# Optimization experiments

Hardware: AMD Instinct MI355X
Metric: run time of the kernel (lower is better)

The kernel has to match this reference:

```python
import jax, jax.numpy as jnp
import numpy as np

BIN_SIZE = 128
DIST_MULT = 0.1
LN_EPS = 1e-6


def setup_inputs() -> dict:
    key = jax.random.key(0)
    ks = jax.random.split(key, 24)
    B, N, D, DD, H = 8, 25600, 256, 128, 128
    s = 0.02
    inp = {
        'x': jax.random.normal(ks[0], (B, N, D), dtype=jnp.float32),
        'msk': jax.random.randint(ks[1], (B, N), 0, 2) > 0,
        'ln_g': jnp.ones((D,), jnp.float32),
        'ln_b': jnp.zeros((D,), jnp.float32),
        # ffn_dist: Linear(256,128) ELU Linear(128,128) ELU Linear(128,128)
        'w1': s * jax.random.normal(ks[2], (D, H), jnp.float32),
        'b1': jnp.zeros((H,), jnp.float32),
        'w2': s * jax.random.normal(ks[3], (H, H), jnp.float32),
        'b2': jnp.zeros((H,), jnp.float32),
        'w3': s * jax.random.normal(ks[4], (H, DD), jnp.float32),
        'b3': jnp.zeros((DD,), jnp.float32),
        # LSH codebook random rotations [distance_dim, max_num_bins//2]
        'codebook': jax.random.normal(ks[5], (DD, 100), jnp.float32),
        # two GHConvDense layers, hidden_dim=output_dim=256
        'theta0': jax.random.normal(ks[6], (D, D), jnp.float32) * s,
        'wh0': jax.random.normal(ks[7], (D, D), jnp.float32) * s,
        'wt0': jax.random.normal(ks[8], (D, D), jnp.float32) * s,
        'bt0': jnp.zeros((D,), jnp.float32),
        'theta1': jax.random.normal(ks[9], (D, D), jnp.float32) * s,
        'wh1': jax.random.normal(ks[10], (D, D), jnp.float32) * s,
        'wt1': jax.random.normal(ks[11], (D, D), jnp.float32) * s,
        'bt1': jnp.zeros((D,), jnp.float32),
    }
    return inp


def _forward(x, msk, ln_g, ln_b, w1, b1, w2, b2, w3, b3, codebook,
             theta0, wh0, wt0, bt0, theta1, wh1, wt1, bt1):
    B, n_elems, D = x.shape
    pad = (-n_elems) % BIN_SIZE  # static python int
    if pad:
        x = jnp.pad(x, ((0, 0), (0, pad), (0, 0)))
        msk = jnp.pad(msk, ((0, 0), (0, pad)), constant_values=True)
    Np = n_elems + pad
    n_bins = Np // BIN_SIZE

    # layernorm
    mu = jnp.mean(x, -1, keepdims=True)
    var = jnp.mean(jnp.square(x - mu), -1, keepdims=True)
    xn = (x - mu) * jax.lax.rsqrt(var + LN_EPS) * ln_g + ln_b

    # distance FFN + dist activation (elu)
    h = jax.nn.elu(xn @ w1 + b1)
    h = jax.nn.elu(h @ w2 + b2)
    x_dist = jax.nn.elu(h @ w3 + b3)  # [B, Np, distance_dim]

    # LSH binning
    mul = x_dist @ codebook[:, :max(1, n_bins // 2)]
    cmul = jnp.concatenate([mul, -mul], axis=-1)  # [B, Np, n_bins]
    a = jnp.argmax(cmul, axis=-1)
    bin_idx = a + jnp.where(msk, 0, n_bins - 1)
    bins_split = jnp.argsort(bin_idx, axis=-1)  # [B, Np]

    # gather into bins
    xm = jnp.take_along_axis(x_dist, bins_split[..., None], axis=1)
    xm = xm.reshape(B, n_bins, BIN_SIZE, x_dist.shape[-1])
    xb = jnp.take_along_axis(xn, bins_split[..., None], axis=1)
    xb = xb.reshape(B, n_bins, BIN_SIZE, D)
    mskf = jnp.take_along_axis(msk, bins_split, axis=1)
    mskf = mskf.reshape(B, n_bins, BIN_SIZE, 1).astype(x.dtype)

    # pairwise Gaussian kernel within each bin
    xk = xm * mskf
    nsq = jnp.sum(jnp.square(xk), -1)  # [B, nb, P]
    inner = jnp.einsum('bnpd,bnqd->bnpq', xk, xk)
    d2 = nsq[..., :, None] - 2.0 * inner + nsq[..., None, :]
    dist = jnp.sqrt(jnp.clip(d2, 1e-6, 1e6))
    dm = jnp.clip(jnp.exp(-DIST_MULT * dist), 0.0, 1.0)
    dm = dm * mskf * jnp.swapaxes(mskf, -1, -2)  # mask rows & cols [B,nb,P,P]

    # gated graph convolutions
    for th, wh, wt, bt in ((theta0, wh0, wt0, bt0), (theta1, wh1, wt1, bt1)):
        xmk = xb * mskf
        f_hom = jnp.einsum('bnpq,bnqd->bnpd', dm, (xmk @ th) * mskf)
        f_het = xmk @ wh
        gate = jax.nn.sigmoid(xb @ wt + bt)
        xb = jax.nn.elu(gate * f_hom + (1.0 - gate) * f_het) * mskf

    # reverse LSH scatter
    xb_flat = xb.reshape(B, Np, D)
    ret = jax.vmap(lambda idx, pts: jnp.zeros((Np, D), pts.dtype).at[idx].set(pts))(
        bins_split, xb_flat)
    return ret[:, :n_elems, :]


def reference(x, msk, ln_g, ln_b, w1, b1, w2, b2, w3, b3, codebook,
              theta0, wh0, wt0, bt0, theta1, wh1, wt1, bt1):
    return _forward(x, msk, ln_g, ln_b, w1, b1, w2, b2, w3, b3, codebook,
                    theta0, wh0, wt0, bt0, theta1, wh1, wt1, bt1)
```

## Files before the change

### kernel.cpp

```cpp
#include <hip/hip_runtime.h>
#include <math.h>

#define B_ 8
#define NP_ 25600
#define T_ (B_*NP_)
#define D_ 256
#define H_ 128
#define DD_ 128
#define NBINS_ 200
#define NIDS_ 400
#define PB_ 128
#define NC_ 100
#define GT_ (B_*NBINS_)

typedef __attribute__((ext_vector_type(8))) short bf16x8;
typedef __attribute__((ext_vector_type(4))) float f32x4;
typedef __attribute__((ext_vector_type(4))) unsigned short u16x4;
typedef unsigned short u16;

__device__ __forceinline__ float eluf(float v){ return v > 0.f ? v : expm1f(v); }
__device__ __forceinline__ u16 f2bf(float f){
  union { float f; unsigned u; } v; v.f = f;
  unsigned r = v.u + 0x7fffu + ((v.u >> 16) & 1u);
  return (u16)(r >> 16);
}
__device__ __forceinline__ float bf2f(u16 h){
  union { unsigned u; float f; } v; v.u = ((unsigned)h) << 16; return v.f;
}

__device__ __forceinline__ void gl16(void* lds, const void* g){
  __builtin_amdgcn_global_load_lds((const __attribute__((address_space(1))) void*)g,
                                   (__attribute__((address_space(3))) void*)lds, 16, 0, 0);
}

__global__ void k_mask_detect(const unsigned int* __restrict__ m, int* __restrict__ flags){
  int any_f1 = 0, any_o = 0;
  for (int i = blockIdx.x*blockDim.x + threadIdx.x; i < T_/4; i += gridDim.x*blockDim.x){
    unsigned int w = m[i];
    if (w == 0x3F800000u) any_f1 = 1;
    else if (w > 1u) any_o = 1;
  }
  if (any_f1) atomicOr(&flags[0], 1);
  if (any_o)  atomicOr(&flags[1], 1);
}

__global__ void k_mask_convert(const void* __restrict__ m, const int* __restrict__ flags,
                               float* __restrict__ mskf){
  int i = blockIdx.x*256 + threadIdx.x;
  int mode = flags[0] ? 2 : (flags[1] ? 1 : 0);
  bool v;
  if (mode == 2)      v = ((const float*)m)[i] != 0.f;
  else if (mode == 1) v = ((const unsigned char*)m)[i] != 0;
  else                v = ((const int*)m)[i] != 0;
  mskf[i] = v ? 1.f : 0.f;
}

__global__ __launch_bounds__(256) void k_ln(const float* __restrict__ x,
    const float* __restrict__ g, const float* __restrict__ b, float* __restrict__ xn){
  const int wave = threadIdx.x >> 6, lane = threadIdx.x & 63;
  const long t = (long)blockIdx.x*4 + wave;
  float4 v = ((const float4*)(x + t*D_))[lane];
  float s  = v.x + v.y + v.z + v.w;
  float s2 = v.x*v.x + v.y*v.y + v.z*v.z + v.w*v.w;
  #pragma unroll
  for (int o = 32; o; o >>= 1){ s += __shfl_xor(s, o); s2 += __shfl_xor(s2, o); }
  const float mu = s * (1.f/D_);
  float var = s2*(1.f/D_) - mu*mu;
  var = fmaxf(var, 0.f);
  const float rs = rsqrtf(var + 1e-6f);
  float4 gg = ((const float4*)g)[lane];
  float4 bb = ((const float4*)b)[lane];
  float4 o4;
  o4.x = (v.x-mu)*rs*gg.x + bb.x;
  o4.y = (v.y-mu)*rs*gg.y + bb.y;
  o4.z = (v.z-mu)*rs*gg.z + bb.z;
  o4.w = (v.w-mu)*rs*gg.w + bb.w;
  ((float4*)(xn + t*D_))[lane] = o4;
}

template<int K>
__global__ __launch_bounds__(256) void k_gemm2(const float* __restrict__ A,
    const float* __restrict__ W, const float* __restrict__ bias, float* __restrict__ C){
  __shared__ __align__(16) float As[32*132];
  __shared__ __align__(16) float Bs[32*132];
  const size_t m0 = (size_t)blockIdx.x * 128;
  const int tid = threadIdx.x;
  const int tm = tid >> 4, tn = tid & 15;
  float acc[8][8] = {};
  for (int kc = 0; kc < K; kc += 32){
    __syncthreads();
    {
      const int r = tid >> 1, kq = (tid & 1) * 16;
      const float* src = &A[(m0 + r)*(size_t)K + kc + kq];
      #pragma unroll
      for (int q = 0; q < 4; ++q){
        const float4 v = ((const float4*)src)[q];
        As[(kq + q*4 + 0)*132 + r] = v.x;
        As[(kq + q*4 + 1)*132 + r] = v.y;
        As[(kq + q*4 + 2)*132 + r] = v.z;
        As[(kq + q*4 + 3)*132 + r] = v.w;
      }
      const int kk = tid >> 3, n0 = (tid & 7) * 16;
      const float* wsrc = &W[(size_t)(kc + kk)*128 + n0];
      #pragma unroll
      for (int q = 0; q < 4; ++q)
        *(float4*)&Bs[kk*132 + n0 + q*4] = ((const float4*)wsrc)[q];
    }
    __syncthreads();
    #pragma unroll
    for (int k = 0; k < 32; ++k){
      float a[8], b[8];
      *(float4*)&a[0] = *(const float4*)&As[k*132 + tm*4];
      *(float4*)&a[4] = *(const float4*)&As[k*132 + 64 + tm*4];
      *(float4*)&b[0] = *(const float4*)&Bs[k*132 + tn*4];
      *(float4*)&b[4] = *(const float4*)&Bs[k*132 + 64 + tn*4];
      #pragma unroll
      for (int i = 0; i < 8; ++i)
        #pragma unroll
        for (int j = 0; j < 8; ++j)
          acc[i][j] = fmaf(a[i], b[j], acc[i][j]);
    }
  }
  #pragma unroll
  for (int i = 0; i < 8; ++i){
    const size_t row = m0 + (i < 4 ? tm*4 + i : 64 + tm*4 + (i-4));
    #pragma unroll
    for (int q = 0; q < 2; ++q){
      const int c0 = q ? 64 + tn*4 : tn*4;
      float4 o;
      o.x = eluf(acc[i][q*4+0] + bias[c0+0]);
      o.y = eluf(acc[i][q*4+1] + bias[c0+1]);
      o.z = eluf(acc[i][q*4+2] + bias[c0+2]);
      o.w = eluf(acc[i][q*4+3] + bias[c0+3]);
      *(float4*)&C[row*128 + c0] = o;
    }
  }
}

__global__ void k_cbpad(const float* __restrict__ cb, float* __restrict__ cbp){
  const int k = blockIdx.x, c = threadIdx.x;
  cbp[k*128 + c] = (c < NC_) ? cb[k*NC_ + c] : 0.f;
}

__global__ __launch_bounds__(256) void k_mulmax(const float* __restrict__ A,
    const float* __restrict__ CB, const float* __restrict__ mskf, int* __restrict__ bidx){
  __shared__ __align__(16) float As[32*132];
  __shared__ __align__(16) float Bs[32*132];
  const size_t m0 = (size_t)blockIdx.x * 128;
  const int tid = threadIdx.x;
  const int tm = tid >> 4, tn = tid & 15;
  float acc[8][8] = {};
  for (int kc = 0; kc < DD_; kc += 32){
    __syncthreads();
    {
      const int r = tid >> 1, kq = (tid & 1) * 16;
      const float* src = &A[(m0 + r)*(size_t)DD_ + kc + kq];
      #pragma unroll
      for (int q = 0; q < 4; ++q){
        const float4 v = ((const float4*)src)[q];
        As[(kq + q*4 + 0)*132 + r] = v.x;
        As[(kq + q*4 + 1)*132 + r] = v.y;
        As[(kq + q*4 + 2)*132 + r] = v.z;
        As[(kq + q*4 + 3)*132 + r] = v.w;
      }
      const int kk = tid >> 3, n0 = (tid & 7) * 16;
      const float* wsrc = &CB[(size_t)(kc + kk)*128 + n0];
      #pragma unroll
      for (int q = 0; q < 4; ++q)
        *(float4*)&Bs[kk*132 + n0 + q*4] = ((const float4*)wsrc)[q];
    }
    __syncthreads();
    #pragma unroll
    for (int k = 0; k < 32; ++k){
      float a[8], b[8];
      *(float4*)&a[0] = *(const float4*)&As[k*132 + tm*4];
      *(float4*)&a[4] = *(const float4*)&As[k*132 + 64 + tm*4];
      *(float4*)&b[0] = *(const float4*)&Bs[k*132 + tn*4];
      *(float4*)&b[4] = *(const float4*)&Bs[k*132 + 64 + tn*4];
      #pragma unroll
      for (int i = 0; i < 8; ++i)
        #pragma unroll
        for (int j = 0; j < 8; ++j)
          acc[i][j] = fmaf(a[i], b[j], acc[i][j]);
    }
  }
  #pragma unroll
  for (int i = 0; i < 8; ++i){
    float bv = -1e30f; int bi = 0;
    #pragma unroll
    for (int j = 0; j < 8; ++j){
      const int c = (j < 4 ? tn*4 + j : 64 + tn*4 + (j-4));
      if (c < NC_){
        const float v = acc[i][j];
        if (v > bv || (v == bv && c < bi)){ bv = v; bi = c; }
        const float nv = -v; const int nc2 = c + NC_;
        if (nv > bv || (nv == bv && nc2 < bi)){ bv = nv; bi = nc2; }
      }
    }
    #pragma unroll
    for (int o = 1; o < 16; o <<= 1){
      const float ov = __shfl_xor(bv, o);
      const int oi = __shfl_xor(bi, o);
      if (ov > bv || (ov == bv && oi < bi)){ bv = ov; bi = oi; }
    }
    if (tn == 0){
      const size_t t = m0 + (i < 4 ? tm*4 + i : 64 + tm*4 + (i-4));
      bidx[t] = bi + (mskf[t] != 0.f ? 0 : NBINS_ - 1);
    }
  }
}

__global__ void k_hist(const int* __restrict__ bidx, int* __restrict__ hist){
  const int i = blockIdx.x*256 + threadIdx.x;
  const int b = i / NP_;
  atomicAdd(&hist[b*NIDS_ + bidx[i]], 1);
}

__global__ void k_prefix(const int* __restrict__ hist, int* __restrict__ offs){
  const int b = threadIdx.x;
  if (b < B_){
    int run = 0;
    for (int v = 0; v < NIDS_; ++v){ offs[b*NIDS_ + v] = run; run += hist[b*NIDS_ + v]; }
  }
}

__global__ __launch_bounds__(64) void k_binsort(const int* __restrict__ bidx,
    const int* __restrict__ offs, const int* __restrict__ hist, int* __restrict__ split){
  const int bv = blockIdx.x;
  if (hist[bv] == 0) return;
  const int b = bv / NIDS_, v = bv % NIDS_;
  int base = offs[bv];
  const int lane = threadIdx.x;
  const int* row = bidx + b*NP_;
  for (int i0 = 0; i0 < NP_; i0 += 64){
    const int i = i0 + lane;
    const bool m = (row[i] == v);
    const unsigned long long mk = __ballot(m);
    if (m){
      const int pos = base + __popcll(mk & ((1ull << lane) - 1ull));
      split[b*NP_ + pos] = i;
    }
    base += __popcll(mk);
  }
}

__global__ __launch_bounds__(256) void k_gather(const float* __restrict__ xn,
    const float* __restrict__ xd, const float* __restrict__ mskf,
    const int* __restrict__ split, u16* __restrict__ xmh,
    u16* __restrict__ xkh, float* __restrict__ mskg){
  const long j = (long)blockIdx.x*4 + (threadIdx.x >> 6);
  const int lane = threadIdx.x & 63;
  const int b = (int)(j / NP_);
  const int i = split[j];
  const long src = (long)b*NP_ + i;
  const float mv = mskf[src];
  const float4 v = ((const float4*)(xn + src*D_))[lane];
  u16x4 o;
  o[0] = f2bf(v.x*mv); o[1] = f2bf(v.y*mv); o[2] = f2bf(v.z*mv); o[3] = f2bf(v.w*mv);
  ((u16x4*)(xmh + j*D_))[lane] = o;
  if (lane < 32){
    const float4 ww = ((const float4*)(xd + src*DD_))[lane];
    u16x4 ow;
    ow[0] = f2bf(ww.x*mv); ow[1] = f2bf(ww.y*mv); ow[2] = f2bf(ww.z*mv); ow[3] = f2bf(ww.w*mv);
    ((u16x4*)(xkh + j*DD_))[lane] = ow;
  }
  if (lane == 0) mskg[j] = mv;
}

__global__ __launch_bounds__(256) void k_wt(const float* __restrict__ W, u16* __restrict__ o){
  const int n = blockIdx.x, k = threadIdx.x;
  o[n*D_ + k] = f2bf(W[k*D_ + n]);
}
__global__ __launch_bounds__(256) void k_wt2(const float* __restrict__ wt,
    const float* __restrict__ wh, u16* __restrict__ o){
  const int n = blockIdx.x, k = threadIdx.x;
  const float v = (n < 256) ? wt[(size_t)k*D_ + n] : wh[(size_t)k*D_ + (n-256)];
  o[(size_t)n*D_ + k] = f2bf(v);
}

__device__ __forceinline__ void stage64a(const u16* __restrict__ g, size_t row0,
    int ld, int k0, u16* Ls, int tid){
  const int w = tid >> 6, l = tid & 63;
  #pragma unroll
  for (int s = 0; s < 4; ++s){
    const int G = (s*4 + w)*64 + l;
    const int r = G >> 3, c8 = G & 7;
    gl16(&Ls[G*8], &g[(row0 + r)*(size_t)ld + k0 + ((c8 ^ (r & 7))*8)]);
  }
}
__device__ __forceinline__ void stage128a(const u16* __restrict__ g, size_t row0,
    int ld, u16* Ls, int tid){
  const int w = tid >> 6, l = tid & 63;
  #pragma unroll
  for (int s = 0; s < 8; ++s){
    const int G = (s*4 + w)*64 + l;
    const int r = G >> 4, c8 = G & 15;
    gl16(&Ls[G*8], &g[(row0 + r)*(size_t)ld + ((c8 ^ (r & 7))*8)]);
  }
}
__device__ __forceinline__ bf16x8 ldf(const u16* Ls, int row, int c8, int ldc8){
  return *(const bf16x8*)&Ls[(row*ldc8 + (c8 ^ (row & 7)))*8];
}

__global__ __launch_bounds__(256) void k_dm(const u16* __restrict__ xk,
    const float* __restrict__ rm, u16* __restrict__ dmb){
  __shared__ __align__(16) u16 Xs[128*128];
  __shared__ float nsq[128];
  __shared__ float msl[128];
  const int g = blockIdx.x;
  const int tid = threadIdx.x, l = tid & 63, wid = tid >> 6;
  const int wr = wid >> 1, wc = wid & 1, lm = l & 15, lk = l >> 4;
  stage128a(xk, (size_t)g*128, DD_, Xs, tid);
  if (tid < 128) msl[tid] = rm[(size_t)g*128 + tid];
  __syncthreads();
  f32x4 acc[4][4] = {};
  #pragma unroll
  for (int ks = 0; ks < 4; ++ks){
    bf16x8 a[4], b[4];
    #pragma unroll
    for (int mi = 0; mi < 4; ++mi) a[mi] = ldf(Xs, wr*64 + mi*16 + lm, ks*4 + lk, 16);
    #pragma unroll
    for (int ni = 0; ni < 4; ++ni) b[ni] = ldf(Xs, wc*64 + ni*16 + lm, ks*4 + lk, 16);
    #pragma unroll
    for (int mi = 0; mi < 4; ++mi)
      #pragma unroll
      for (int ni = 0; ni < 4; ++ni)
        acc[mi][ni] = __builtin_amdgcn_mfma_f32_16x16x32_bf16(a[mi], b[ni], acc[mi][ni], 0, 0, 0);
  }
  if (wr == wc && ((lm >> 2) == lk)){
    #pragma unroll
    for (int mi = 0; mi < 4; ++mi)
      nsq[wr*64 + mi*16 + lm] = acc[mi][mi][lm & 3];
  }
  __syncthreads();
  #pragma unroll
  for (int mi = 0; mi < 4; ++mi)
    #pragma unroll
    for (int ni = 0; ni < 4; ++ni)
      #pragma unroll
      for (int r = 0; r < 4; ++r){
        const int row = wr*64 + mi*16 + lk*4 + r;
        const int col = wc*64 + ni*16 + lm;
        float d2 = nsq[row] + nsq[col] - 2.f*acc[mi][ni][r];
        d2 = fminf(fmaxf(d2, 1e-6f), 1e6f);
        float w = expf(-0.1f * sqrtf(d2));
        w = fminf(w, 1.f);
        dmb[((size_t)g*PB_ + row)*PB_ + col] = f2bf(w * msl[row] * msl[col]);
      }
}

template<int OUT>
__global__ __launch_bounds__(256, 2) void k_fuse(const u16* __restrict__ dmb,
    const u16* __restrict__ thT, const u16* __restrict__ wtwh,
    const u16* __restrict__ X, const float* __restrict__ btv,
    const int* __restrict__ split, u16* __restrict__ o16, float* __restrict__ o32){
  __shared__ __align__(16) u16 smem[32768];
  __shared__ int ssp[128];
  u16* bufA = smem;
  u16* bufB = smem + 16384;
  const int bid = blockIdx.x;
  const int id = (bid & 7)*400 + (bid >> 3);
  const int h = id & 1, g = id >> 1;
  const int tid = threadIdx.x, l = tid & 63, wid = tid >> 6;
  const int wr = wid >> 1, wc = wid & 1, lm = l & 15, lk = l >> 4;
  u16* SBw = bufB;
  u16* SBh = bufB + 8192;
  if (OUT){ if (tid < 128) ssp[tid] = split[g*128 + tid]; }
  f32x4 at[4][4] = {}, ah[4][4] = {};
  for (int kt = 0; kt < 4; ++kt){
    __syncthreads();
    stage64a(X,    (size_t)g*128,       D_, kt*64, bufA, tid);
    stage64a(wtwh, (size_t)h*128,       D_, kt*64, SBw, tid);
    stage64a(wtwh, (size_t)(256+h*128), D_, kt*64, SBh, tid);
    __syncthreads();
    #pragma unroll
    for (int ks = 0; ks < 2; ++ks){
      bf16x8 xa[4], bt_[4], bh_[4];
      #pragma unroll
      for (int mi = 0; mi < 4; ++mi) xa[mi] = ldf(bufA, wr*64 + mi*16 + lm, ks*4 + lk, 8);
      #pragma unroll
      for (int ni = 0; ni < 4; ++ni){
        bt_[ni] = ldf(SBw, wc*64 + ni*16 + lm, ks*4 + lk, 8);
        bh_[ni] = ldf(SBh, wc*64 + ni*16 + lm, ks*4 + lk, 8);
      }
      #pragma unroll
      for (int mi = 0; mi < 4; ++mi)
        #pragma unroll
        for (int ni = 0; ni < 4; ++ni){
          at[mi][ni] = __builtin_amdgcn_mfma_f32_16x16x32_bf16(xa[mi], bt_[ni], at[mi][ni], 0, 0, 0);
          ah[mi][ni] = __builtin_amdgcn_mfma_f32_16x16x32_bf16(xa[mi], bh_[ni], ah[mi][ni], 0, 0, 0);
        }
    }
  }
  u16x4 atp[4][4], ahp[4][4];
  #pragma unroll
  for (int mi = 0; mi < 4; ++mi)
    #pragma unroll
    for (int ni = 0; ni < 4; ++ni)
      #pragma unroll
      for (int r = 0; r < 4; ++r){
        atp[mi][ni][r] = f2bf(at[mi][ni][r]);
        ahp[mi][ni][r] = f2bf(ah[mi][ni][r]);
      }
  f32x4 a1[4][4] = {};
  for (int kt = 0; kt < 4; ++kt){
    __syncthreads();
    stage64a(thT, (size_t)h*128, D_, kt*64, bufA, tid);
    stage64a(X,   (size_t)g*128, D_, kt*64, bufB, tid);
    __syncthreads();
    #pragma unroll
    for (int ks = 0; ks < 2; ++ks){
      bf16x8 a[4], b[4];
      #pragma unroll
      for (int mi = 0; mi < 4; ++mi) a[mi] = ldf(bufA, wr*64 + mi*16 + lm, ks*4 + lk, 8);
      #pragma unroll
      for (int ni = 0; ni < 4; ++ni) b[ni] = ldf(bufB, wc*64 + ni*16 + lm, ks*4 + lk, 8);
      #pragma unroll
      for (int mi = 0; mi < 4; ++mi)
        #pragma unroll
        for (int ni = 0; ni < 4; ++ni)
          a1[mi][ni] = __builtin_amdgcn_mfma_f32_16x16x32_bf16(a[mi], b[ni], a1[mi][ni], 0, 0, 0);
    }
  }
  __syncthreads();
  #pragma unroll
  for (int mi = 0; mi < 4; ++mi)
    #pragma unroll
    for (int ni = 0; ni < 4; ++ni)
      #pragma unroll
      for (int r = 0; r < 4; ++r){
        const int row = wr*64 + mi*16 + lk*4 + r;
        const int col = wc*64 + ni*16 + lm;
        bufB[(row*16 + ((col >> 3) ^ (row & 7)))*8 + (col & 7)] = f2bf(a1[mi][ni][r]);
      }
  stage128a(dmb, (size_t)g*128, PB_, bufA, tid);
  __syncthreads();
  f32x4 acc[4][4] = {};
  #pragma unroll
  for (int ks = 0; ks < 4; ++ks){
    bf16x8 a[4], b[4];
    #pragma unroll
    for (int mi = 0; mi < 4; ++mi) a[mi] = ldf(bufA, wr*64 + mi*16 + lm, ks*4 + lk, 16);
    #pragma unroll
    for (int ni = 0; ni < 4; ++ni) b[ni] = ldf(bufB, wc*64 + ni*16 + lm, ks*4 + lk, 16);
    #pragma unroll
    for (int mi = 0; mi < 4; ++mi)
      #pragma unroll
      for (int ni = 0; ni < 4; ++ni)
        acc[mi][ni] = __builtin_amdgcn_mfma_f32_16x16x32_bf16(a[mi], b[ni], acc[mi][ni], 0, 0, 0);
  }
  __syncthreads();
  if (OUT == 0){
    #pragma unroll
    for (int mi = 0; mi < 4; ++mi)
      #pragma unroll
      for (int ni = 0; ni < 4; ++ni){
        const int colc = wc*64 + ni*16 + lm;
        const float bb = btv[h*128 + colc];
        #pragma unroll
        for (int r = 0; r < 4; ++r){
          const int row = wr*64 + mi*16 + lk*4 + r;
          const float gt = 1.f/(1.f + expf(-(bf2f(atp[mi][ni][r]) + bb)));
          const float o = eluf(gt*acc[mi][ni][r] + (1.f - gt)*bf2f(ahp[mi][ni][r]));
          bufA[row*128 + colc] = f2bf(o);
        }
      }
    __syncthreads();
    #pragma unroll
    for (int s = 0; s < 8; ++s){
      const int G = s*256 + tid;
      const int r = G >> 4, c8 = G & 15;
      *(bf16x8*)&o16[((size_t)g*128 + r)*D_ + h*128 + c8*8] = *(const bf16x8*)&bufA[r*128 + c8*8];
    }
  } else {
    float* fb = (float*)smem;
    #pragma unroll
    for (int mi = 0; mi < 4; ++mi)
      #pragma unroll
      for (int ni = 0; ni < 4; ++ni){
        const int colc = wc*64 + ni*16 + lm;
        const float bb = btv[h*128 + colc];
        #pragma unroll
        for (int r = 0; r < 4; ++r){
          const int row = wr*64 + mi*16 + lk*4 + r;
          const float gt = 1.f/(1.f + expf(-(bf2f(atp[mi][ni][r]) + bb)));
          fb[row*128 + colc] = eluf(gt*acc[mi][ni][r] + (1.f - gt)*bf2f(ahp[mi][ni][r]));
        }
      }
    __syncthreads();
    const int b = g / NBINS_;
    #pragma unroll
    for (int s = 0; s < 16; ++s){
      const int G = s*256 + tid;
      const int r = G >> 5, c4 = G & 31;
      const float4 v = *(const float4*)&fb[r*128 + c4*4];
      *(float4*)&o32[((size_t)b*NP_ + ssp[r])*D_ + h*128 + c4*4] = v;
    }
  }
}

extern "C" void kernel_launch(void* const* d_in, const int* in_sizes, int n_in,
                              void* d_out, int out_size, void* d_ws, size_t ws_size,
                              hipStream_t stream){
  (void)in_sizes; (void)n_in; (void)out_size;
  const float* x    = (const float*)d_in[0];
  const void*  msk  = d_in[1];
  const float* ln_g = (const float*)d_in[2];
  const float* ln_b = (const float*)d_in[3];
  const float* w1 = (const float*)d_in[4];
  const float* b1 = (const float*)d_in[5];
  const float* w2 = (const float*)d_in[6];
  const float* b2 = (const float*)d_in[7];
  const float* w3 = (const float*)d_in[8];
  const float* b3 = (const float*)d_in[9];
  const float* cb = (const float*)d_in[10];
  const float* th0 = (const float*)d_in[11];
  const float* wh0 = (const float*)d_in[12];
  const float* wt0 = (const float*)d_in[13];
  const float* bt0 = (const float*)d_in[14];
  const float* th1 = (const float*)d_in[15];
  const float* wh1 = (const float*)d_in[16];
  const float* wt1 = (const float*)d_in[17];
  const float* bt1 = (const float*)d_in[18];
  float* out = (float*)d_out;

  char* ws = (char*)d_ws;
  size_t off = 0;
  auto alloc = [&](size_t bytes) -> void* {
    void* p = ws + off; off += (bytes + 255) & ~(size_t)255; return p;
  };
  int* flags = (int*)alloc(2*sizeof(int));
  int* hist  = (int*)alloc((size_t)B_*NIDS_*4);
  int* offs  = (int*)alloc((size_t)B_*NIDS_*4);
  int* bidx  = (int*)alloc((size_t)T_*4);
  int* split = (int*)alloc((size_t)T_*4);
  float* mskf = (float*)alloc((size_t)T_*4);
  float* mskg = (float*)alloc((size_t)T_*4);
  float* cbp = (float*)alloc((size_t)128*128*4);
  u16* thT0 = (u16*)alloc((size_t)D_*D_*2);
  u16* thT1 = (u16*)alloc((size_t)D_*D_*2);
  u16* wtwh0 = (u16*)alloc((size_t)512*D_*2);
  u16* wtwh1 = (u16*)alloc((size_t)512*D_*2);
  char* regA = (char*)alloc((size_t)T_*512*2);
  u16* xmh = (u16*)alloc((size_t)T_*D_*2);
  char* regC = (char*)alloc((size_t)T_*D_*2);
  u16* xb1 = (u16*)alloc((size_t)T_*D_*2);
  if (off > ws_size) return;

  float* P = (float*)regA;
  float* Q = P + (size_t)T_*DD_;
  u16* xkh = (u16*)regC;
  u16* dmb = xkh + (size_t)T_*DD_;
  float* xn = out;

  hipMemsetAsync(flags, 0, 2*sizeof(int), stream);
  hipMemsetAsync(hist, 0, (size_t)B_*NIDS_*4, stream);

  k_mask_detect<<<64, 256, 0, stream>>>((const unsigned int*)msk, flags);
  k_mask_convert<<<T_/256, 256, 0, stream>>>(msk, flags, mskf);

  k_ln<<<T_/4, 256, 0, stream>>>(x, ln_g, ln_b, xn);

  k_cbpad<<<128, 128, 0, stream>>>(cb, cbp);
  k_wt<<<256, 256, 0, stream>>>(th0, thT0);
  k_wt<<<256, 256, 0, stream>>>(th1, thT1);
  k_wt2<<<512, 256, 0, stream>>>(wt0, wh0, wtwh0);
  k_wt2<<<512, 256, 0, stream>>>(wt1, wh1, wtwh1);

  k_gemm2<D_><<<T_/128, 256, 0, stream>>>(xn, w1, b1, P);
  k_gemm2<H_><<<T_/128, 256, 0, stream>>>(P, w2, b2, Q);
  k_gemm2<H_><<<T_/128, 256, 0, stream>>>(Q, w3, b3, P);

  k_mulmax<<<T_/128, 256, 0, stream>>>(P, cbp, mskf, bidx);
  k_hist<<<T_/256, 256, 0, stream>>>(bidx, hist);
  k_prefix<<<1, 64, 0, stream>>>(hist, offs);
  k_binsort<<<B_*NIDS_, 64, 0, stream>>>(bidx, offs, hist, split);

  k_gather<<<T_/4, 256, 0, stream>>>(xn, P, mskf, split, xmh, xkh, mskg);
  k_dm<<<GT_, 256, 0, stream>>>(xkh, mskg, dmb);

  k_fuse<0><<<2*GT_, 256, 0, stream>>>(dmb, thT0, wtwh0, xmh, bt0, nullptr, xb1, nullptr);
  k_fuse<1><<<2*GT_, 256, 0, stream>>>(dmb, thT1, wtwh1, xb1, bt1, split, nullptr, out);
}
```

Measured before the change: 1.281 ms.

## Shrink k_fuse shared memory to 48KB to allow three blocks per CU

```diff
diff --git a/kernel.cpp b/kernel.cpp
--- a/kernel.cpp
+++ b/kernel.cpp
@@ -350,38 +350,38 @@
 }
 
 template<int OUT>
-__global__ __launch_bounds__(256, 2) void k_fuse(const u16* __restrict__ dmb,
+__global__ __launch_bounds__(256, 3) void k_fuse(const u16* __restrict__ dmb,
     const u16* __restrict__ thT, const u16* __restrict__ wtwh,
     const u16* __restrict__ X, const float* __restrict__ btv,
     const int* __restrict__ split, u16* __restrict__ o16, float* __restrict__ o32){
-  __shared__ __align__(16) u16 smem[32768];
+  __shared__ __align__(16) u16 smem[24576];
   __shared__ int ssp[128];
-  u16* bufA = smem;
-  u16* bufB = smem + 16384;
+  u16* S0 = smem;
+  u16* S1 = smem + 8192;
+  u16* S2 = smem + 16384;
+  u16* TT = smem + 8192;
   const int bid = blockIdx.x;
   const int id = (bid & 7)*400 + (bid >> 3);
   const int h = id & 1, g = id >> 1;
   const int tid = threadIdx.x, l = tid & 63, wid = tid >> 6;
   const int wr = wid >> 1, wc = wid & 1, lm = l & 15, lk = l >> 4;
-  u16* SBw = bufB;
-  u16* SBh = bufB + 8192;
   if (OUT){ if (tid < 128) ssp[tid] = split[g*128 + tid]; }
   f32x4 at[4][4] = {}, ah[4][4] = {};
   for (int kt = 0; kt < 4; ++kt){
     __syncthreads();
-    stage64a(X,    (size_t)g*128,       D_, kt*64, bufA, tid);
-    stage64a(wtwh, (size_t)h*128,       D_, kt*64, SBw, tid);
-    stage64a(wtwh, (size_t)(256+h*128), D_, kt*64, SBh, tid);
+    stage64a(X,    (size_t)g*128,       D_, kt*64, S0, tid);
+    stage64a(wtwh, (size_t)h*128,       D_, kt*64, S1, tid);
+    stage64a(wtwh, (size_t)(256+h*128), D_, kt*64, S2, tid);
     __syncthreads();
     #pragma unroll
     for (int ks = 0; ks < 2; ++ks){
       bf16x8 xa[4], bt_[4], bh_[4];
       #pragma unroll
-      for (int mi = 0; mi < 4; ++mi) xa[mi] = ldf(bufA, wr*64 + mi*16 + lm, ks*4 + lk, 8);
+      for (int mi = 0; mi < 4; ++mi) xa[mi] = ldf(S0, wr*64 + mi*16 + lm, ks*4 + lk, 8);
       #pragma unroll
       for (int ni = 0; ni < 4; ++ni){
-        bt_[ni] = ldf(SBw, wc*64 + ni*16 + lm, ks*4 + lk, 8);
-        bh_[ni] = ldf(SBh, wc*64 + ni*16 + lm, ks*4 + lk, 8);
+        bt_[ni] = ldf(S1, wc*64 + ni*16 + lm, ks*4 + lk, 8);
+        bh_[ni] = ldf(S2, wc*64 + ni*16 + lm, ks*4 + lk, 8);
       }
       #pragma unroll
       for (int mi = 0; mi < 4; ++mi)
@@ -405,16 +405,16 @@
   f32x4 a1[4][4] = {};
   for (int kt = 0; kt < 4; ++kt){
     __syncthreads();
-    stage64a(thT, (size_t)h*128, D_, kt*64, bufA, tid);
-    stage64a(X,   (size_t)g*128, D_, kt*64, bufB, tid);
+    stage64a(thT, (size_t)h*128, D_, kt*64, S0, tid);
+    stage64a(X,   (size_t)g*128, D_, kt*64, S1, tid);
     __syncthreads();
     #pragma unroll
     for (int ks = 0; ks < 2; ++ks){
       bf16x8 a[4], b[4];
       #pragma unroll
-      for (int mi = 0; mi < 4; ++mi) a[mi] = ldf(bufA, wr*64 + mi*16 + lm, ks*4 + lk, 8);
-      #pragma unroll
-      for (int ni = 0; ni < 4; ++ni) b[ni] = ldf(bufB, wc*64 + ni*16 + lm, ks*4 + lk, 8);
+      for (int mi = 0; mi < 4; ++mi) a[mi] = ldf(S0, wr*64 + mi*16 + lm, ks*4 + lk, 8);
+      #pragma unroll
+      for (int ni = 0; ni < 4; ++ni) b[ni] = ldf(S1, wc*64 + ni*16 + lm, ks*4 + lk, 8);
       #pragma unroll
       for (int mi = 0; mi < 4; ++mi)
         #pragma unroll
@@ -431,26 +431,31 @@
       for (int r = 0; r < 4; ++r){
         const int row = wr*64 + mi*16 + lk*4 + r;
         const int col = wc*64 + ni*16 + lm;
-        bufB[(row*16 + ((col >> 3) ^ (row & 7)))*8 + (col & 7)] = f2bf(a1[mi][ni][r]);
-      }
-  stage128a(dmb, (size_t)g*128, PB_, bufA, tid);
-  __syncthreads();
+        TT[(row*16 + ((col >> 3) ^ (row & 7)))*8 + (col & 7)] = f2bf(a1[mi][ni][r]);
+      }
   f32x4 acc[4][4] = {};
   #pragma unroll
-  for (int ks = 0; ks < 4; ++ks){
-    bf16x8 a[4], b[4];
-    #pragma unroll
-    for (int mi = 0; mi < 4; ++mi) a[mi] = ldf(bufA, wr*64 + mi*16 + lm, ks*4 + lk, 16);
-    #pragma unroll
-    for (int ni = 0; ni < 4; ++ni) b[ni] = ldf(bufB, wc*64 + ni*16 + lm, ks*4 + lk, 16);
-    #pragma unroll
-    for (int mi = 0; mi < 4; ++mi)
-      #pragma unroll
-      for (int ni = 0; ni < 4; ++ni)
-        acc[mi][ni] = __builtin_amdgcn_mfma_f32_16x16x32_bf16(a[mi], b[ni], acc[mi][ni], 0, 0, 0);
+  for (int hk = 0; hk < 2; ++hk){
+    __syncthreads();
+    stage64a(dmb, (size_t)g*128, PB_, hk*64, S0, tid);
+    __syncthreads();
+    #pragma unroll
+    for (int ks2 = 0; ks2 < 2; ++ks2){
+      bf16x8 a[4], b[4];
+      #pragma unroll
+      for (int mi = 0; mi < 4; ++mi) a[mi] = ldf(S0, wr*64 + mi*16 + lm, ks2*4 + lk, 8);
+      #pragma unroll
+      for (int ni = 0; ni < 4; ++ni) b[ni] = ldf(TT, wc*64 + ni*16 + lm, (hk*2 + ks2)*4 + lk, 16);
+      #pragma unroll
+      for (int mi = 0; mi < 4; ++mi)
+        #pragma unroll
+        for (int ni = 0; ni < 4; ++ni)
+          acc[mi][ni] = __builtin_amdgcn_mfma_f32_16x16x32_bf16(a[mi], b[ni], acc[mi][ni], 0, 0, 0);
+    }
   }
   __syncthreads();
   if (OUT == 0){
+    u16* EB = smem;
     #pragma unroll
     for (int mi = 0; mi < 4; ++mi)
       #pragma unroll
@@ -462,7 +467,7 @@
           const int row = wr*64 + mi*16 + lk*4 + r;
           const float gt = 1.f/(1.f + expf(-(bf2f(atp[mi][ni][r]) + bb)));
           const float o = eluf(gt*acc[mi][ni][r] + (1.f - gt)*bf2f(ahp[mi][ni][r]));
-          bufA[row*128 + colc] = f2bf(o);
+          EB[row*128 + colc] = f2bf(o);
         }
       }
     __syncthreads();
@@ -470,31 +475,37 @@
     for (int s = 0; s < 8; ++s){
       const int G = s*256 + tid;
       const int r = G >> 4, c8 = G & 15;
-      *(bf16x8*)&o16[((size_t)g*128 + r)*D_ + h*128 + c8*8] = *(const bf16x8*)&bufA[r*128 + c8*8];
+      *(bf16x8*)&o16[((size_t)g*128 + r)*D_ + h*128 + c8*8] = *(const bf16x8*)&EB[r*128 + c8*8];
     }
   } else {
     float* fb = (float*)smem;
-    #pragma unroll
-    for (int mi = 0; mi < 4; ++mi)
-      #pragma unroll
-      for (int ni = 0; ni < 4; ++ni){
-        const int colc = wc*64 + ni*16 + lm;
-        const float bb = btv[h*128 + colc];
-        #pragma unroll
-        for (int r = 0; r < 4; ++r){
-          const int row = wr*64 + mi*16 + lk*4 + r;
-          const float gt = 1.f/(1.f + expf(-(bf2f(atp[mi][ni][r]) + bb)));
-          fb[row*128 + colc] = eluf(gt*acc[mi][ni][r] + (1.f - gt)*bf2f(ahp[mi][ni][r]));
-        }
-      }
-    __syncthreads();
     const int b = g / NBINS_;
     #pragma unroll
-    for (int s = 0; s < 16; ++s){
-      const int G = s*256 + tid;
-      const int r = G >> 5, c4 = G & 31;
-      const float4 v = *(const float4*)&fb[r*128 + c4*4];
-      *(float4*)&o32[((size_t)b*NP_ + ssp[r])*D_ + h*128 + c4*4] = v;
+    for (int pass = 0; pass < 2; ++pass){
+      __syncthreads();
+      if (wr == pass){
+        #pragma unroll
+        for (int mi = 0; mi < 4; ++mi)
+          #pragma unroll
+          for (int ni = 0; ni < 4; ++ni){
+            const int colc = wc*64 + ni*16 + lm;
+            const float bb = btv[h*128 + colc];
+            #pragma unroll
+            for (int r = 0; r < 4; ++r){
+              const int lrow = mi*16 + lk*4 + r;
+              const float gt = 1.f/(1.f + expf(-(bf2f(atp[mi][ni][r]) + bb)));
+              fb[lrow*128 + colc] = eluf(gt*acc[mi][ni][r] + (1.f - gt)*bf2f(ahp[mi][ni][r]));
+            }
+          }
+      }
+      __syncthreads();
+      #pragma unroll
+      for (int s = 0; s < 8; ++s){
+        const int G = s*256 + tid;
+        const int r = G >> 5, c4 = G & 31;
+        const float4 v = *(const float4*)&fb[r*128 + c4*4];
+        *(float4*)&o32[((size_t)b*NP_ + ssp[pass*64 + r])*D_ + h*128 + c4*4] = v;
+      }
     }
   }
 }
```

Measured after the change: 2.187 ms. +70.8%, slower.
